# Optimization experiments

Measured on AMD Instinct MI355X. Metric: run time of the kernel, lower is better.

Reference implementation:

```python
import jax, jax.numpy as jnp
import numpy as np

NX = NY = 2048
DT = 0.01
DX = 1.0
DY = 1.0
RE = 1.0
NLEVEL = int(np.log2(NY)) + 1  # 12 levels


def pad_zero(x):
    # Dirichlet (zero) halo of width 1: matches boundary_condition_u/v/k/cw
    return jnp.pad(x, ((0, 0), (0, 0), (1, 1), (1, 1)))


def pad_edge(x):
    # Edge-replicate halo (incl. corners): matches boundary_condition_p
    return jnp.pad(x, ((0, 0), (0, 0), (1, 1), (1, 1)), mode='edge')


def conv2d(x, w, stride=1):
    return jax.lax.conv_general_dilated(
        x, w, (stride, stride), 'VALID',
        dimension_numbers=('NCHW', 'OIHW', 'NCHW'))


def upsample2(x):
    return jnp.repeat(jnp.repeat(x, 2, axis=2), 2, axis=3)


def pg_vector(u, v, pad_u, pad_v, k1, ADx_u, ADy_u, ADx_v, ADy_v, AD2_u, AD2_v, w_diff):
    # Petrov-Galerkin dissipation. pad_u/pad_v are the padded ORIGINAL velocities:
    # the torch code references the global values_uu/values_vv buffers here.
    k_u = 0.25 * DX * jnp.abs(0.5 * DX ** -3 * (jnp.abs(u) * DX + jnp.abs(v) * DY) * AD2_u) \
        / (0.001 + (jnp.abs(ADx_u) * DX ** -3 + jnp.abs(ADy_u) * DX ** -3) / 2.0)
    k_v = 0.25 * DY * jnp.abs(0.5 * DX ** -3 * (jnp.abs(u) * DX + jnp.abs(v) * DY) * AD2_v) \
        / (0.001 + (jnp.abs(ADx_v) * DX ** -3 + jnp.abs(ADy_v) * DX ** -3) / 2.0)
    k_u = jnp.minimum(k_u, k1)
    k_v = jnp.minimum(k_v, k1)
    k_uu = pad_zero(k_u)
    k_vv = pad_zero(k_v)
    k_x = 1.5 * (k_u * AD2_u + conv2d(pad_u * k_uu, w_diff) - u * conv2d(k_uu, w_diff))
    k_y = 1.5 * (k_v * AD2_v + conv2d(pad_v * k_vv, w_diff) - v * conv2d(k_vv, w_diff))
    return k_x, k_y


def f_cycle_mg(pad_u, pad_v, values_p, iteration, w_A, w_res, w_xadv, w_yadv):
    diag = w_A[0, 0, 1, 1]
    b = -(conv2d(pad_u, w_xadv) + conv2d(pad_v, w_yadv)) / DT
    w = jnp.zeros((1, 1, 2, 2), values_p.dtype)
    r = b
    for _ in range(iteration):
        w = jnp.zeros((1, 1, 2, 2), values_p.dtype)
        r = conv2d(pad_edge(values_p), w_A) - b
        r_s = [r]
        for _i in range(1, NLEVEL - 1):
            r = conv2d(r, w_res, stride=2)  # restriction down to 2x2
            r_s.append(r)
        for i in reversed(range(1, NLEVEL - 1)):
            w = w - conv2d(pad_zero(w), w_A) / diag + r_s[i] / diag  # Jacobi smooth
            w = upsample2(w)  # prolongation
        values_p = values_p - w
        values_p = values_p - conv2d(pad_edge(values_p), w_A) / diag + b / diag
    return values_p, w, r


def setup_inputs() -> dict:
    key = jax.random.key(0)
    ku, kv, kp = jax.random.split(key, 3)
    shp = (1, 1, NY, NX)
    f32 = jnp.float32
    values_u = jax.random.normal(ku, shp, f32) * 0.1
    values_v = jax.random.normal(kv, shp, f32) * 0.1
    values_p = jax.random.normal(kp, shp, f32) * 0.1
    Fx = jnp.zeros(shp, f32)
    Fy = jnp.zeros(shp, f32)
    k1 = jnp.ones(shp, f32) * (DX ** 2 / DT)
    # FD stencils (learned conv params in the torch module)
    w_xadv = jnp.array([[0., 0., 0.], [-0.5, 0., 0.5], [0., 0., 0.]], f32).reshape(1, 1, 3, 3) / DX
    w_yadv = jnp.array([[0., -0.5, 0.], [0., 0., 0.], [0., 0.5, 0.]], f32).reshape(1, 1, 3, 3) / DY
    lap = jnp.array([[0., 1., 0.], [1., -4., 1.], [0., 1., 0.]], f32).reshape(1, 1, 3, 3) / DX ** 2
    w_diff = lap
    w_A = lap  # diag = -4
    w_res = jnp.full((1, 1, 2, 2), 0.25, f32)
    return dict(values_u=values_u, values_v=values_v, values_p=values_p,
                Fx=Fx, Fy=Fy, k1=k1,
                w_xadv=w_xadv, w_yadv=w_yadv, w_diff=w_diff, w_A=w_A, w_res=w_res,
                iteration=5)


def reference(values_u, values_v, values_p, Fx, Fy, k1,
              w_xadv, w_yadv, w_diff, w_A, w_res, iteration):
    pad_u = pad_zero(values_u)
    pad_v = pad_zero(values_v)
    pad_p = pad_edge(values_p)
    Grapx_p = conv2d(pad_p, w_xadv) * DT
    Grapy_p = conv2d(pad_p, w_yadv) * DT
    ADx_u = conv2d(pad_u, w_xadv); ADy_u = conv2d(pad_u, w_yadv)
    ADx_v = conv2d(pad_v, w_xadv); ADy_v = conv2d(pad_v, w_yadv)
    AD2_u = conv2d(pad_u, w_diff); AD2_v = conv2d(pad_v, w_diff)
    k_x, k_y = pg_vector(values_u, values_v, pad_u, pad_v, k1,
                         ADx_u, ADy_u, ADx_v, ADy_v, AD2_u, AD2_v, w_diff)
    b_u = values_u + 0.5 * (RE * k_x * DT - values_u * ADx_u * DT - values_v * ADy_u * DT) - Grapx_p - Fx * DT * 0
    b_v = values_v + 0.5 * (RE * k_y * DT - values_u * ADx_v * DT - values_v * ADy_v * DT) - Grapy_p - Fy * DT * 0
    pad_bu = pad_zero(b_u)
    pad_bv = pad_zero(b_v)
    ADx_u = conv2d(pad_bu, w_xadv); ADy_u = conv2d(pad_bu, w_yadv)
    ADx_v = conv2d(pad_bv, w_xadv); ADy_v = conv2d(pad_bv, w_yadv)
    AD2_u = conv2d(pad_bu, w_diff); AD2_v = conv2d(pad_bv, w_diff)
    # torch code closes over the global padded ORIGINAL velocities here (pad_u, pad_v)
    k_x, k_y = pg_vector(b_u, b_v, pad_u, pad_v, k1,
                         ADx_u, ADy_u, ADx_v, ADy_v, AD2_u, AD2_v, w_diff)
    values_u = values_u + RE * k_x * DT - b_u * ADx_u * DT - b_v * ADy_u * DT - Grapx_p - Fx * DT
    values_v = values_v + RE * k_y * DT - b_u * ADx_v * DT - b_v * ADy_v * DT - Grapy_p - Fy * DT
    values_p, w, r = f_cycle_mg(pad_zero(values_u), pad_zero(values_v), values_p,
                                iteration, w_A, w_res, w_xadv, w_yadv)
    pad_p2 = pad_edge(values_p)
    values_u = values_u - conv2d(pad_p2, w_xadv) * DT
    values_v = values_v - conv2d(pad_p2, w_yadv) * DT
    return values_u, values_v, values_p, w, r
```

## Files before the change

kernel.cpp:

```cpp
#include <hip/hip_runtime.h>

#define NN 2048
#define NN2 (NN * NN)

__device__ __forceinline__ void load6z(const float* __restrict__ A, int i, int j0, float a[6]) {
    if ((unsigned)i >= (unsigned)NN) {
#pragma unroll
        for (int q = 0; q < 6; ++q) a[q] = 0.f;
        return;
    }
    const float* row = A + (size_t)i * NN;
    float4 c = *reinterpret_cast<const float4*>(row + j0);
    a[1] = c.x; a[2] = c.y; a[3] = c.z; a[4] = c.w;
    a[0] = (j0 > 0) ? row[j0 - 1] : 0.f;
    a[5] = (j0 + 4 < NN) ? row[j0 + 4] : 0.f;
}
__device__ __forceinline__ void load4z(const float* __restrict__ A, int i, int j0, float a[4]) {
    if ((unsigned)i >= (unsigned)NN) {
#pragma unroll
        for (int q = 0; q < 4; ++q) a[q] = 0.f;
        return;
    }
    float4 c = *reinterpret_cast<const float4*>(A + (size_t)i * NN + j0);
    a[0] = c.x; a[1] = c.y; a[2] = c.z; a[3] = c.w;
}
__device__ __forceinline__ void load6e(const float* __restrict__ A, int i, int j0, float a[6]) {
    i = i < 0 ? 0 : (i > NN - 1 ? NN - 1 : i);
    const float* row = A + (size_t)i * NN;
    float4 c = *reinterpret_cast<const float4*>(row + j0);
    a[1] = c.x; a[2] = c.y; a[3] = c.z; a[4] = c.w;
    a[0] = (j0 > 0) ? row[j0 - 1] : c.x;
    a[5] = (j0 + 4 < NN) ? row[j0 + 4] : c.w;
}
__device__ __forceinline__ void load4e(const float* __restrict__ A, int i, int j0, float a[4]) {
    i = i < 0 ? 0 : (i > NN - 1 ? NN - 1 : i);
    float4 c = *reinterpret_cast<const float4*>(A + (size_t)i * NN + j0);
    a[0] = c.x; a[1] = c.y; a[2] = c.z; a[3] = c.w;
}
__device__ __forceinline__ void store4(float* __restrict__ A, int i, int j0, const float a[4]) {
    *reinterpret_cast<float4*>(A + (size_t)i * NN + j0) = make_float4(a[0], a[1], a[2], a[3]);
}

__global__ __launch_bounds__(256) void k_pg1_v(const float* __restrict__ u, const float* __restrict__ v,
                                               const float* __restrict__ k1,
                                               float* __restrict__ ku, float* __restrict__ kv) {
    int jt = blockIdx.x * blockDim.x + threadIdx.x;
    int i  = blockIdx.y * blockDim.y + threadIdx.y;
    int j0 = jt * 4;
    float u6[6], v6[6], uu[4], ud[4], vu[4], vd[4], kc[4], oku[4], okv[4];
    load6z(u, i, j0, u6); load6z(v, i, j0, v6);
    load4z(u, i - 1, j0, uu); load4z(u, i + 1, j0, ud);
    load4z(v, i - 1, j0, vu); load4z(v, i + 1, j0, vd);
    load4z(k1, i, j0, kc);
#pragma unroll
    for (int c = 0; c < 4; ++c) {
        float uc = u6[c + 1], ul = u6[c], ur = u6[c + 2], ut = uu[c], ub = ud[c];
        float vc = v6[c + 1], vl = v6[c], vr = v6[c + 2], vt = vu[c], vb = vd[c];
        float ADxu = 0.5f * (ur - ul), ADyu = 0.5f * (ub - ut);
        float ADxv = 0.5f * (vr - vl), ADyv = 0.5f * (vb - vt);
        float Lu = ul + ur + ut + ub - 4.f * uc;
        float Lv = vl + vr + vt + vb - 4.f * vc;
        float s = fabsf(uc) + fabsf(vc);
        float kuv = 0.25f * fabsf(0.5f * s * Lu) / (0.001f + 0.5f * (fabsf(ADxu) + fabsf(ADyu)));
        float kvv = 0.25f * fabsf(0.5f * s * Lv) / (0.001f + 0.5f * (fabsf(ADxv) + fabsf(ADyv)));
        oku[c] = fminf(kuv, kc[c]); okv[c] = fminf(kvv, kc[c]);
    }
    store4(ku, i, j0, oku); store4(kv, i, j0, okv);
}

__global__ __launch_bounds__(256) void k_pred_v(const float* __restrict__ u, const float* __restrict__ v,
                                                const float* __restrict__ p,
                                                const float* __restrict__ ku, const float* __restrict__ kv,
                                                float* __restrict__ bu, float* __restrict__ bv) {
    const float DT = 0.01f;
    int jt = blockIdx.x * blockDim.x + threadIdx.x;
    int i  = blockIdx.y * blockDim.y + threadIdx.y;
    int j0 = jt * 4;
    float u6[6], v6[6], uu[4], ud[4], vu[4], vd[4];
    float ku6[6], kv6[6], kuu[4], kud[4], kvu[4], kvd[4];
    float p6[6], pu[4], pd[4], obu[4], obv[4];
    load6z(u, i, j0, u6); load6z(v, i, j0, v6);
    load4z(u, i - 1, j0, uu); load4z(u, i + 1, j0, ud);
    load4z(v, i - 1, j0, vu); load4z(v, i + 1, j0, vd);
    load6z(ku, i, j0, ku6); load6z(kv, i, j0, kv6);
    load4z(ku, i - 1, j0, kuu); load4z(ku, i + 1, j0, kud);
    load4z(kv, i - 1, j0, kvu); load4z(kv, i + 1, j0, kvd);
    load6e(p, i, j0, p6); load4e(p, i - 1, j0, pu); load4e(p, i + 1, j0, pd);
#pragma unroll
    for (int c = 0; c < 4; ++c) {
        float uc = u6[c + 1], ul = u6[c], ur = u6[c + 2], ut = uu[c], ub = ud[c];
        float vc = v6[c + 1], vl = v6[c], vr = v6[c + 2], vt = vu[c], vb = vd[c];
        float kuc = ku6[c + 1], kul = ku6[c], kur = ku6[c + 2], kut = kuu[c], kub = kud[c];
        float kvc = kv6[c + 1], kvl = kv6[c], kvr = kv6[c + 2], kvt = kvu[c], kvb = kvd[c];
        float ADxu = 0.5f * (ur - ul), ADyu = 0.5f * (ub - ut);
        float ADxv = 0.5f * (vr - vl), ADyv = 0.5f * (vb - vt);
        float Lu = ul + ur + ut + ub - 4.f * uc;
        float Lv = vl + vr + vt + vb - 4.f * vc;
        float Lku = kul + kur + kut + kub - 4.f * kuc;
        float Lkv = kvl + kvr + kvt + kvb - 4.f * kvc;
        float Luku = ul * kul + ur * kur + ut * kut + ub * kub - 4.f * uc * kuc;
        float Lvkv = vl * kvl + vr * kvr + vt * kvt + vb * kvb - 4.f * vc * kvc;
        float kx = 1.5f * (kuc * Lu + Luku - uc * Lku);
        float ky = 1.5f * (kvc * Lv + Lvkv - vc * Lkv);
        float Grapx = 0.5f * (p6[c + 2] - p6[c]) * DT;
        float Grapy = 0.5f * (pd[c] - pu[c]) * DT;
        obu[c] = uc + 0.5f * (kx * DT - uc * ADxu * DT - vc * ADyu * DT) - Grapx;
        obv[c] = vc + 0.5f * (ky * DT - uc * ADxv * DT - vc * ADyv * DT) - Grapy;
    }
    store4(bu, i, j0, obu); store4(bv, i, j0, obv);
}

__global__ __launch_bounds__(256) void k_corr_v(const float* __restrict__ u, const float* __restrict__ v,
                                                const float* __restrict__ p,
                                                const float* __restrict__ bu, const float* __restrict__ bv,
                                                const float* __restrict__ ku, const float* __restrict__ kv,
                                                const float* __restrict__ Fx, const float* __restrict__ Fy,
                                                float* __restrict__ un, float* __restrict__ vn) {
    const float DT = 0.01f;
    int jt = blockIdx.x * blockDim.x + threadIdx.x;
    int i  = blockIdx.y * blockDim.y + threadIdx.y;
    int j0 = jt * 4;
    float u6[6], v6[6], uu[4], ud[4], vu[4], vd[4];
    float bu6[6], bv6[6], buu[4], bud[4], bvu[4], bvd[4];
    float ku6[6], kv6[6], kuu[4], kud[4], kvu[4], kvd[4];
    float p6[6], pu[4], pd[4], fx[4], fy[4], oun[4], ovn[4];
    load6z(u, i, j0, u6); load6z(v, i, j0, v6);
    load4z(u, i - 1, j0, uu); load4z(u, i + 1, j0, ud);
    load4z(v, i - 1, j0, vu); load4z(v, i + 1, j0, vd);
    load6z(bu, i, j0, bu6); load6z(bv, i, j0, bv6);
    load4z(bu, i - 1, j0, buu); load4z(bu, i + 1, j0, bud);
    load4z(bv, i - 1, j0, bvu); load4z(bv, i + 1, j0, bvd);
    load6z(ku, i, j0, ku6); load6z(kv, i, j0, kv6);
    load4z(ku, i - 1, j0, kuu); load4z(ku, i + 1, j0, kud);
    load4z(kv, i - 1, j0, kvu); load4z(kv, i + 1, j0, kvd);
    load6e(p, i, j0, p6); load4e(p, i - 1, j0, pu); load4e(p, i + 1, j0, pd);
    load4z(Fx, i, j0, fx); load4z(Fy, i, j0, fy);
#pragma unroll
    for (int c = 0; c < 4; ++c) {
        float uc = u6[c + 1], ul = u6[c], ur = u6[c + 2], ut = uu[c], ub = ud[c];
        float vc = v6[c + 1], vl = v6[c], vr = v6[c + 2], vt = vu[c], vb = vd[c];
        float buc = bu6[c + 1], bul = bu6[c], bur = bu6[c + 2], but = buu[c], bub = bud[c];
        float bvc = bv6[c + 1], bvl = bv6[c], bvr = bv6[c + 2], bvt = bvu[c], bvb = bvd[c];
        float kuc = ku6[c + 1], kul = ku6[c], kur = ku6[c + 2], kut = kuu[c], kub = kud[c];
        float kvc = kv6[c + 1], kvl = kv6[c], kvr = kv6[c + 2], kvt = kvu[c], kvb = kvd[c];
        float ADxbu = 0.5f * (bur - bul), ADybu = 0.5f * (bub - but);
        float ADxbv = 0.5f * (bvr - bvl), ADybv = 0.5f * (bvb - bvt);
        float Lbu = bul + bur + but + bub - 4.f * buc;
        float Lbv = bvl + bvr + bvt + bvb - 4.f * bvc;
        float Lku = kul + kur + kut + kub - 4.f * kuc;
        float Lkv = kvl + kvr + kvt + kvb - 4.f * kvc;
        float Luku = ul * kul + ur * kur + ut * kut + ub * kub - 4.f * uc * kuc;
        float Lvkv = vl * kvl + vr * kvr + vt * kvt + vb * kvb - 4.f * vc * kvc;
        float kx = 1.5f * (kuc * Lbu + Luku - buc * Lku);
        float ky = 1.5f * (kvc * Lbv + Lvkv - bvc * Lkv);
        float Grapx = 0.5f * (p6[c + 2] - p6[c]) * DT;
        float Grapy = 0.5f * (pd[c] - pu[c]) * DT;
        oun[c] = uc + kx * DT - buc * ADxbu * DT - bvc * ADybu * DT - Grapx - fx[c] * DT;
        ovn[c] = vc + ky * DT - buc * ADxbv * DT - bvc * ADybv * DT - Grapy - fy[c] * DT;
    }
    store4(un, i, j0, oun); store4(vn, i, j0, ovn);
}

__global__ __launch_bounds__(256) void k_rhs_v(const float* __restrict__ un, const float* __restrict__ vn,
                                               float* __restrict__ b) {
    const float INVDT = 100.0f;
    int jt = blockIdx.x * blockDim.x + threadIdx.x;
    int i  = blockIdx.y * blockDim.y + threadIdx.y;
    int j0 = jt * 4;
    float u6[6], vu[4], vd[4], ob[4];
    load6z(un, i, j0, u6);
    load4z(vn, i - 1, j0, vu); load4z(vn, i + 1, j0, vd);
#pragma unroll
    for (int c = 0; c < 4; ++c) {
        float adx = 0.5f * (u6[c + 2] - u6[c]);
        float ady = 0.5f * (vd[c] - vu[c]);
        ob[c] = -(adx + ady) * INVDT;
    }
    store4(b, i, j0, ob);
}

__global__ __launch_bounds__(256) void k_resrestrict(const float* __restrict__ p, const float* __restrict__ b,
                                                     float* __restrict__ r1024, float* __restrict__ r512) {
    int jt = blockIdx.x * blockDim.x + threadIdx.x;
    int it = blockIdx.y * blockDim.y + threadIdx.y;
    int j0 = jt * 4, i0 = it * 4;
    float p6[6][6];
#pragma unroll
    for (int r = 0; r < 6; ++r) load6e(p, i0 - 1 + r, j0, p6[r]);
    float res[4][4];
#pragma unroll
    for (int r = 0; r < 4; ++r) {
        float bb[4];
        load4z(b, i0 + r, j0, bb);
#pragma unroll
        for (int c = 0; c < 4; ++c) {
            float pc = p6[r + 1][c + 1];
            float nb = p6[r][c + 1] + p6[r + 2][c + 1] + p6[r + 1][c] + p6[r + 1][c + 2];
            res[r][c] = nb - 4.f * pc - bb[c];
        }
    }
    float q00 = 0.25f * (res[0][0] + res[0][1] + res[1][0] + res[1][1]);
    float q01 = 0.25f * (res[0][2] + res[0][3] + res[1][2] + res[1][3]);
    float q10 = 0.25f * (res[2][0] + res[2][1] + res[3][0] + res[3][1]);
    float q11 = 0.25f * (res[2][2] + res[2][3] + res[3][2] + res[3][3]);
    int ci = it * 2, cj = jt * 2;
    *reinterpret_cast<float2*>(r1024 + (size_t)ci * 1024 + cj)       = make_float2(q00, q01);
    *reinterpret_cast<float2*>(r1024 + (size_t)(ci + 1) * 1024 + cj) = make_float2(q10, q11);
    r512[(size_t)it * 512 + jt] = 0.25f * (q00 + q01 + q10 + q11);
}

__global__ __launch_bounds__(256) void k_restrict2(const float* __restrict__ src,
                                                   float* __restrict__ dst1, float* __restrict__ dst2,
                                                   int n_src) {
    int j = blockIdx.x * blockDim.x + threadIdx.x;
    int i = blockIdx.y * blockDim.y + threadIdx.y;
    int n4 = n_src >> 2;
    int n2 = n_src >> 1;
    const float4* r0 = reinterpret_cast<const float4*>(src + (4 * i + 0) * n_src + 4 * j);
    const float4* r1 = reinterpret_cast<const float4*>(src + (4 * i + 1) * n_src + 4 * j);
    const float4* r2 = reinterpret_cast<const float4*>(src + (4 * i + 2) * n_src + 4 * j);
    const float4* r3 = reinterpret_cast<const float4*>(src + (4 * i + 3) * n_src + 4 * j);
    float4 a0 = *r0, a1 = *r1, a2 = *r2, a3 = *r3;
    float s00 = a0.x + a0.y + a1.x + a1.y;
    float s01 = a0.z + a0.w + a1.z + a1.w;
    float s10 = a2.x + a2.y + a3.x + a3.y;
    float s11 = a2.z + a2.w + a3.z + a3.w;
    *reinterpret_cast<float2*>(dst1 + (2 * i) * n2 + 2 * j)     = make_float2(0.25f * s00, 0.25f * s01);
    *reinterpret_cast<float2*>(dst1 + (2 * i + 1) * n2 + 2 * j) = make_float2(0.25f * s10, 0.25f * s11);
    dst2[i * n4 + j] = 0.0625f * (s00 + s01 + s10 + s11);
}

__global__ __launch_bounds__(1024) void k_small(const float* __restrict__ r128,
                                                float* __restrict__ w128_out,
                                                float* __restrict__ r2_out) {
    __shared__ float sr64[64 * 64];
    __shared__ float sr32[32 * 32];
    __shared__ float sr16[16 * 16];
    __shared__ float sr8[8 * 8];
    __shared__ float sr4[16];
    __shared__ float sr2[4];
    __shared__ float wa[64 * 64];
    __shared__ float wb[64 * 64];
    int t = threadIdx.x;

    for (int idx = t; idx < 64 * 64; idx += 1024) {
        int i = idx >> 6, j = idx & 63;
        const float* s0 = r128 + (2 * i) * 128 + 2 * j;
        sr64[idx] = 0.25f * (s0[0] + s0[1] + s0[128] + s0[129]);
    }
    __syncthreads();
    if (t < 32 * 32) {
        int i = t >> 5, j = t & 31;
        const float* s0 = sr64 + (2 * i) * 64 + 2 * j;
        sr32[t] = 0.25f * (s0[0] + s0[1] + s0[64] + s0[65]);
    }
    __syncthreads();
    if (t < 16 * 16) {
        int i = t >> 4, j = t & 15;
        const float* s0 = sr32 + (2 * i) * 32 + 2 * j;
        sr16[t] = 0.25f * (s0[0] + s0[1] + s0[32] + s0[33]);
    }
    __syncthreads();
    if (t < 64) {
        int i = t >> 3, j = t & 7;
        const float* s0 = sr16 + (2 * i) * 16 + 2 * j;
        sr8[t] = 0.25f * (s0[0] + s0[1] + s0[16] + s0[17]);
    }
    __syncthreads();
    if (t < 16) {
        int i = t >> 2, j = t & 3;
        const float* s0 = sr8 + (2 * i) * 8 + 2 * j;
        sr4[t] = 0.25f * (s0[0] + s0[1] + s0[8] + s0[9]);
    }
    __syncthreads();
    if (t < 4) {
        int i = t >> 1, j = t & 1;
        const float* s0 = sr4 + (2 * i) * 4 + 2 * j;
        sr2[t] = 0.25f * (s0[0] + s0[1] + s0[4] + s0[5]);
        r2_out[t] = sr2[t];
        float ws = -0.25f * sr2[t];
        wa[(2 * i) * 4 + 2 * j] = ws;
        wa[(2 * i) * 4 + 2 * j + 1] = ws;
        wa[(2 * i + 1) * 4 + 2 * j] = ws;
        wa[(2 * i + 1) * 4 + 2 * j + 1] = ws;
    }
    __syncthreads();

    auto step = [&](const float* win, const float* rl, float* wout, int s) {
        for (int idx = t; idx < s * s; idx += 1024) {
            int i = idx / s, j = idx - i * s;
            float up = i > 0 ? win[(i - 1) * s + j] : 0.f;
            float dn = i < s - 1 ? win[(i + 1) * s + j] : 0.f;
            float lf = j > 0 ? win[i * s + j - 1] : 0.f;
            float rt = j < s - 1 ? win[i * s + j + 1] : 0.f;
            float ws = 0.25f * (up + dn + lf + rt - rl[idx]);
            int o = 2 * s;
            wout[(2 * i) * o + 2 * j] = ws;
            wout[(2 * i) * o + 2 * j + 1] = ws;
            wout[(2 * i + 1) * o + 2 * j] = ws;
            wout[(2 * i + 1) * o + 2 * j + 1] = ws;
        }
    };
    step(wa, sr4, wb, 4);
    __syncthreads();
    step(wb, sr8, wa, 8);
    __syncthreads();
    step(wa, sr16, wb, 16);
    __syncthreads();
    step(wb, sr32, wa, 32);
    __syncthreads();
    step(wa, sr64, w128_out, 64);
}

__global__ __launch_bounds__(256) void k_prolong(const float* __restrict__ win, const float* __restrict__ rl,
                                                 float* __restrict__ wout, int n) {
    int j = blockIdx.x * blockDim.x + threadIdx.x;
    int i = blockIdx.y * blockDim.y + threadIdx.y;
    float up = i > 0 ? win[(i - 1) * n + j] : 0.f;
    float dn = i < n - 1 ? win[(i + 1) * n + j] : 0.f;
    float lf = j > 0 ? win[i * n + j - 1] : 0.f;
    float rt = j < n - 1 ? win[i * n + j + 1] : 0.f;
    float ws = 0.25f * (up + dn + lf + rt - rl[i * n + j]);
    int o = 2 * n;
    float2 vv = make_float2(ws, ws);
    *reinterpret_cast<float2*>(wout + (2 * i) * o + 2 * j) = vv;
    *reinterpret_cast<float2*>(wout + (2 * i + 1) * o + 2 * j) = vv;
}

template <bool LAST>
__global__ __launch_bounds__(256) void k_pupd_f(const float* __restrict__ p, const float* __restrict__ b,
                                                const float* __restrict__ w1024, const float* __restrict__ r1024,
                                                float* __restrict__ pdst, float* __restrict__ wout) {
    __shared__ float ws[4][130];
    const int jb = blockIdx.x * 256;
    const int ib = blockIdx.y * 4;
    const int cr_base = ib / 2 - 1;
    const int cc_base = jb / 2 - 1;
    const int tid = threadIdx.y * 64 + threadIdx.x;

    for (int cell = tid; cell < 4 * 130; cell += 256) {
        int r = cell / 130, c = cell - r * 130;
        int ci = cr_base + r, cj = cc_base + c;
        float val = 0.f;
        if ((unsigned)ci < 1024u && (unsigned)cj < 1024u) {
            const float* wr = w1024 + (size_t)ci * 1024;
            float up = ci > 0    ? wr[cj - 1024] : 0.f;
            float dn = ci < 1023 ? wr[cj + 1024] : 0.f;
            float lf = cj > 0    ? wr[cj - 1] : 0.f;
            float rt = cj < 1023 ? wr[cj + 1] : 0.f;
            val = 0.25f * (up + dn + lf + rt - r1024[(size_t)ci * 1024 + cj]);
        }
        ws[r][c] = val;
    }
    __syncthreads();

    const int i  = ib + threadIdx.y;
    const int j0 = jb + threadIdx.x * 4;
    float p6[6], pu[4], pd[4], bb[4], op[4];
    load6e(p, i, j0, p6);
    load4e(p, i - 1, j0, pu);
    load4e(p, i + 1, j0, pd);
    load4z(b, i, j0, bb);

    const int iu = (i - 1) < 0 ? 0 : (i - 1);
    const int id = (i + 1) > NN - 1 ? NN - 1 : (i + 1);
    const int lrC = (i >> 1) - cr_base;
    const int lrU = (iu >> 1) - cr_base;
    const int lrD = (id >> 1) - cr_base;

#pragma unroll
    for (int c = 0; c < 4; ++c) {
        int f = j0 + c;
        int fl = (f - 1) < 0 ? 0 : (f - 1);
        int fr = (f + 1) > NN - 1 ? NN - 1 : (f + 1);
        float pml = p6[c]     - ws[lrC][(fl >> 1) - cc_base];
        float pmr = p6[c + 2] - ws[lrC][(fr >> 1) - cc_base];
        float pmt = pu[c]     - ws[lrU][(f >> 1) - cc_base];
        float pmb = pd[c]     - ws[lrD][(f >> 1) - cc_base];
        op[c] = 0.25f * (pml + pmr + pmt + pmb - bb[c]);
    }
    store4(pdst, i, j0, op);
    if (LAST) {
        float ow[4];
#pragma unroll
        for (int c = 0; c < 4; ++c) ow[c] = ws[lrC][((j0 + c) >> 1) - cc_base];
        store4(wout, i, j0, ow);
    }
}

__global__ __launch_bounds__(256) void k_fcorr_v(const float* __restrict__ p,
                                                 float* __restrict__ un, float* __restrict__ vn) {
    const float DT = 0.01f;
    int jt = blockIdx.x * blockDim.x + threadIdx.x;
    int i  = blockIdx.y * blockDim.y + threadIdx.y;
    int j0 = jt * 4;
    float p6[6], pu[4], pd[4];
    load6e(p, i, j0, p6);
    load4e(p, i - 1, j0, pu);
    load4e(p, i + 1, j0, pd);
    float4 uc = *reinterpret_cast<float4*>(un + (size_t)i * NN + j0);
    float4 vc = *reinterpret_cast<float4*>(vn + (size_t)i * NN + j0);
    float ou[4] = {uc.x, uc.y, uc.z, uc.w};
    float ov[4] = {vc.x, vc.y, vc.z, vc.w};
#pragma unroll
    for (int c = 0; c < 4; ++c) {
        ou[c] -= 0.5f * (p6[c + 2] - p6[c]) * DT;
        ov[c] -= 0.5f * (pd[c] - pu[c]) * DT;
    }
    store4(un, i, j0, ou);
    store4(vn, i, j0, ov);
}

extern "C" void kernel_launch(void* const* d_in, const int* in_sizes, int n_in,
                              void* d_out, int out_size, void* d_ws, size_t ws_size,
                              hipStream_t stream) {
    const float* u  = (const float*)d_in[0];
    const float* v  = (const float*)d_in[1];
    const float* p  = (const float*)d_in[2];
    const float* Fx = (const float*)d_in[3];
    const float* Fy = (const float*)d_in[4];
    const float* k1 = (const float*)d_in[5];

    float* out = (float*)d_out;
    float* out_u = out;
    float* out_v = out + (size_t)NN2;
    float* out_p = out + 2 * (size_t)NN2;
    float* out_w = out + 3 * (size_t)NN2;
    float* out_r = out + 4 * (size_t)NN2;

    float* ws = (float*)d_ws;
    float* ku = ws;
    float* kv = ws + (size_t)NN2;
    float* b  = ws + 2 * (size_t)NN2;
    float* pA = ws + 3 * (size_t)NN2;
    float* pB = kv;
    float* r1024 = ws + 4 * (size_t)NN2;
    float* r512  = r1024 + 1024 * 1024;
    float* r256  = r512 + 512 * 512;
    float* r128  = r256 + 256 * 256;
    float* w128  = r128 + 128 * 128;
    float* w256  = w128 + 128 * 128;
    float* w512  = w256 + 256 * 256;
    float* w1024 = w512 + 512 * 512;

    float* bu = out_w;
    float* bv = out_p;

    dim3 blk(64, 4);
    dim3 g4(8, 512);

    k_pg1_v<<<g4, blk, 0, stream>>>(u, v, k1, ku, kv);
    k_pred_v<<<g4, blk, 0, stream>>>(u, v, p, ku, kv, bu, bv);
    k_pg1_v<<<g4, blk, 0, stream>>>(bu, bv, k1, ku, kv);
    k_corr_v<<<g4, blk, 0, stream>>>(u, v, p, bu, bv, ku, kv, Fx, Fy, out_u, out_v);
    k_rhs_v<<<g4, blk, 0, stream>>>(out_u, out_v, b);

    const float* pcur = p;
    for (int it = 0; it < 5; ++it) {
        k_resrestrict<<<dim3(8, 128), blk, 0, stream>>>(pcur, b, r1024, r512);
        k_restrict2<<<dim3(2, 32), blk, 0, stream>>>(r512, r256, r128, 512);
        k_small<<<1, 1024, 0, stream>>>(r128, w128, out_r);
        k_prolong<<<dim3(2, 32), blk, 0, stream>>>(w128, r128, w256, 128);
        k_prolong<<<dim3(4, 64), blk, 0, stream>>>(w256, r256, w512, 256);
        k_prolong<<<dim3(8, 128), blk, 0, stream>>>(w512, r512, w1024, 512);
        if (it < 4) {
            float* pdst = (it & 1) ? pB : pA;
            k_pupd_f<false><<<dim3(8, 512), blk, 0, stream>>>(pcur, b, w1024, r1024, pdst, nullptr);
            pcur = pdst;
        } else {
            k_pupd_f<true><<<dim3(8, 512), blk, 0, stream>>>(pcur, b, w1024, r1024, out_p, out_w);
        }
    }

    k_fcorr_v<<<g4, blk, 0, stream>>>(out_p, out_u, out_v);
}
```

Measured before the change: 425.7 us.

## Fuse PG dissipation into predictor/corrector and fold restriction and prolongation levels

Merges the two k_pg1 passes into the predictor and corrector kernels. Each block computes the limited diffusivity on a haloed shared-memory tile, so ku/kv no longer make a round trip through global memory. The 512→256→128 restriction is folded into the residual-restriction kernel using shared-memory reductions. The finest prolongation level is recomputed inside the pressure-update kernel from w512 and r512, removing the w1024 buffer. Together this drops several full-grid launches per cycle, at the cost of redundant halo computation, more shared memory per block and extra __syncthreads barriers.

```diff
diff --git a/kernel.cpp b/kernel.cpp
--- a/kernel.cpp
+++ b/kernel.cpp
@@ -41,124 +41,204 @@
     *reinterpret_cast<float4*>(A + (size_t)i * NN + j0) = make_float4(a[0], a[1], a[2], a[3]);
 }
 
-__global__ __launch_bounds__(256) void k_pg1_v(const float* __restrict__ u, const float* __restrict__ v,
-                                               const float* __restrict__ k1,
-                                               float* __restrict__ ku, float* __restrict__ kv) {
-    int jt = blockIdx.x * blockDim.x + threadIdx.x;
-    int i  = blockIdx.y * blockDim.y + threadIdx.y;
-    int j0 = jt * 4;
-    float u6[6], v6[6], uu[4], ud[4], vu[4], vd[4], kc[4], oku[4], okv[4];
-    load6z(u, i, j0, u6); load6z(v, i, j0, v6);
-    load4z(u, i - 1, j0, uu); load4z(u, i + 1, j0, ud);
-    load4z(v, i - 1, j0, vu); load4z(v, i + 1, j0, vd);
-    load4z(k1, i, j0, kc);
-#pragma unroll
-    for (int c = 0; c < 4; ++c) {
-        float uc = u6[c + 1], ul = u6[c], ur = u6[c + 2], ut = uu[c], ub = ud[c];
-        float vc = v6[c + 1], vl = v6[c], vr = v6[c + 2], vt = vu[c], vb = vd[c];
-        float ADxu = 0.5f * (ur - ul), ADyu = 0.5f * (ub - ut);
-        float ADxv = 0.5f * (vr - vl), ADyv = 0.5f * (vb - vt);
-        float Lu = ul + ur + ut + ub - 4.f * uc;
-        float Lv = vl + vr + vt + vb - 4.f * vc;
-        float s = fabsf(uc) + fabsf(vc);
-        float kuv = 0.25f * fabsf(0.5f * s * Lu) / (0.001f + 0.5f * (fabsf(ADxu) + fabsf(ADyu)));
-        float kvv = 0.25f * fabsf(0.5f * s * Lv) / (0.001f + 0.5f * (fabsf(ADxv) + fabsf(ADyv)));
-        oku[c] = fminf(kuv, kc[c]); okv[c] = fminf(kvv, kc[c]);
-    }
-    store4(ku, i, j0, oku); store4(kv, i, j0, okv);
-}
-
-__global__ __launch_bounds__(256) void k_pred_v(const float* __restrict__ u, const float* __restrict__ v,
-                                                const float* __restrict__ p,
-                                                const float* __restrict__ ku, const float* __restrict__ kv,
+__global__ __launch_bounds__(256) void k_pred_f(const float* __restrict__ u, const float* __restrict__ v,
+                                                const float* __restrict__ k1, const float* __restrict__ p,
                                                 float* __restrict__ bu, float* __restrict__ bv) {
     const float DT = 0.01f;
-    int jt = blockIdx.x * blockDim.x + threadIdx.x;
-    int i  = blockIdx.y * blockDim.y + threadIdx.y;
-    int j0 = jt * 4;
-    float u6[6], v6[6], uu[4], ud[4], vu[4], vd[4];
-    float ku6[6], kv6[6], kuu[4], kud[4], kvu[4], kvd[4];
-    float p6[6], pu[4], pd[4], obu[4], obv[4];
-    load6z(u, i, j0, u6); load6z(v, i, j0, v6);
-    load4z(u, i - 1, j0, uu); load4z(u, i + 1, j0, ud);
-    load4z(v, i - 1, j0, vu); load4z(v, i + 1, j0, vd);
-    load6z(ku, i, j0, ku6); load6z(kv, i, j0, kv6);
-    load4z(ku, i - 1, j0, kuu); load4z(ku, i + 1, j0, kud);
-    load4z(kv, i - 1, j0, kvu); load4z(kv, i + 1, j0, kvd);
-    load6e(p, i, j0, p6); load4e(p, i - 1, j0, pu); load4e(p, i + 1, j0, pd);
-#pragma unroll
-    for (int c = 0; c < 4; ++c) {
-        float uc = u6[c + 1], ul = u6[c], ur = u6[c + 2], ut = uu[c], ub = ud[c];
-        float vc = v6[c + 1], vl = v6[c], vr = v6[c + 2], vt = vu[c], vb = vd[c];
-        float kuc = ku6[c + 1], kul = ku6[c], kur = ku6[c + 2], kut = kuu[c], kub = kud[c];
-        float kvc = kv6[c + 1], kvl = kv6[c], kvr = kv6[c + 2], kvt = kvu[c], kvb = kvd[c];
-        float ADxu = 0.5f * (ur - ul), ADyu = 0.5f * (ub - ut);
-        float ADxv = 0.5f * (vr - vl), ADyv = 0.5f * (vb - vt);
-        float Lu = ul + ur + ut + ub - 4.f * uc;
-        float Lv = vl + vr + vt + vb - 4.f * vc;
-        float Lku = kul + kur + kut + kub - 4.f * kuc;
-        float Lkv = kvl + kvr + kvt + kvb - 4.f * kvc;
-        float Luku = ul * kul + ur * kur + ut * kut + ub * kub - 4.f * uc * kuc;
-        float Lvkv = vl * kvl + vr * kvr + vt * kvt + vb * kvb - 4.f * vc * kvc;
-        float kx = 1.5f * (kuc * Lu + Luku - uc * Lku);
-        float ky = 1.5f * (kvc * Lv + Lvkv - vc * Lkv);
-        float Grapx = 0.5f * (p6[c + 2] - p6[c]) * DT;
-        float Grapy = 0.5f * (pd[c] - pu[c]) * DT;
-        obu[c] = uc + 0.5f * (kx * DT - uc * ADxu * DT - vc * ADyu * DT) - Grapx;
-        obv[c] = vc + 0.5f * (ky * DT - uc * ADxv * DT - vc * ADyv * DT) - Grapy;
-    }
-    store4(bu, i, j0, obu); store4(bv, i, j0, obv);
-}
-
-__global__ __launch_bounds__(256) void k_corr_v(const float* __restrict__ u, const float* __restrict__ v,
-                                                const float* __restrict__ p,
+    __shared__ __align__(16) float su[36][72], sv[36][72];
+    __shared__ float sku[34][68], skv[34][68];
+    const int jb = blockIdx.x * 64;
+    const int ib = blockIdx.y * 32;
+    const int tid = threadIdx.y * 16 + threadIdx.x;
+
+    for (int idx = tid; idx < 36 * 18; idx += 256) {
+        int r = idx / 18, c4 = idx - r * 18;
+        int gi = ib - 2 + r;
+        int gj = jb - 4 + c4 * 4;
+        float4 uu = make_float4(0.f, 0.f, 0.f, 0.f), vv = uu;
+        if ((unsigned)gi < (unsigned)NN) {
+            if (gj >= 0 && gj + 3 < NN) {
+                uu = *reinterpret_cast<const float4*>(u + (size_t)gi * NN + gj);
+                vv = *reinterpret_cast<const float4*>(v + (size_t)gi * NN + gj);
+            } else {
+                float tu[4], tv[4];
+#pragma unroll
+                for (int q = 0; q < 4; ++q) {
+                    int g = gj + q;
+                    bool in = (unsigned)g < (unsigned)NN;
+                    tu[q] = in ? u[(size_t)gi * NN + g] : 0.f;
+                    tv[q] = in ? v[(size_t)gi * NN + g] : 0.f;
+                }
+                uu = make_float4(tu[0], tu[1], tu[2], tu[3]);
+                vv = make_float4(tv[0], tv[1], tv[2], tv[3]);
+            }
+        }
+        *reinterpret_cast<float4*>(&su[r][c4 * 4]) = uu;
+        *reinterpret_cast<float4*>(&sv[r][c4 * 4]) = vv;
+    }
+    __syncthreads();
+
+    for (int idx = tid; idx < 34 * 66; idx += 256) {
+        int r = idx / 66, c = idx - r * 66;
+        int gi = ib - 1 + r, gj = jb - 1 + c;
+        float kuo = 0.f, kvo = 0.f;
+        if ((unsigned)gi < (unsigned)NN && (unsigned)gj < (unsigned)NN) {
+            int lr = r + 1, lc = c + 3;
+            float uc = su[lr][lc], ul = su[lr][lc - 1], ur = su[lr][lc + 1], ut = su[lr - 1][lc], ub = su[lr + 1][lc];
+            float vc = sv[lr][lc], vl = sv[lr][lc - 1], vr = sv[lr][lc + 1], vt = sv[lr - 1][lc], vb = sv[lr + 1][lc];
+            float ADxu = 0.5f * (ur - ul), ADyu = 0.5f * (ub - ut);
+            float ADxv = 0.5f * (vr - vl), ADyv = 0.5f * (vb - vt);
+            float Lu = ul + ur + ut + ub - 4.f * uc;
+            float Lv = vl + vr + vt + vb - 4.f * vc;
+            float s = fabsf(uc) + fabsf(vc);
+            float kuv = 0.25f * fabsf(0.5f * s * Lu) / (0.001f + 0.5f * (fabsf(ADxu) + fabsf(ADyu)));
+            float kvv = 0.25f * fabsf(0.5f * s * Lv) / (0.001f + 0.5f * (fabsf(ADxv) + fabsf(ADyv)));
+            float k1c = k1[(size_t)gi * NN + gj];
+            kuo = fminf(kuv, k1c);
+            kvo = fminf(kvv, k1c);
+        }
+        sku[r][c] = kuo;
+        skv[r][c] = kvo;
+    }
+    __syncthreads();
+
+    const int i0 = ib + threadIdx.y * 2;
+    const int j0 = jb + threadIdx.x * 4;
+#pragma unroll
+    for (int a = 0; a < 2; ++a) {
+        int i = i0 + a;
+        float p6[6], pu[4], pd[4], obu[4], obv[4];
+        load6e(p, i, j0, p6); load4e(p, i - 1, j0, pu); load4e(p, i + 1, j0, pd);
+        int lur = i - ib + 2, lkr = i - ib + 1;
+#pragma unroll
+        for (int c = 0; c < 4; ++c) {
+            int luc = j0 + c - jb + 4, lkc = j0 + c - jb + 1;
+            float uc = su[lur][luc], ul = su[lur][luc - 1], ur = su[lur][luc + 1], ut = su[lur - 1][luc], ub = su[lur + 1][luc];
+            float vc = sv[lur][luc], vl = sv[lur][luc - 1], vr = sv[lur][luc + 1], vt = sv[lur - 1][luc], vb = sv[lur + 1][luc];
+            float kuc = sku[lkr][lkc], kul = sku[lkr][lkc - 1], kur = sku[lkr][lkc + 1], kut = sku[lkr - 1][lkc], kub = sku[lkr + 1][lkc];
+            float kvc = skv[lkr][lkc], kvl = skv[lkr][lkc - 1], kvr = skv[lkr][lkc + 1], kvt = skv[lkr - 1][lkc], kvb = skv[lkr + 1][lkc];
+            float ADxu = 0.5f * (ur - ul), ADyu = 0.5f * (ub - ut);
+            float ADxv = 0.5f * (vr - vl), ADyv = 0.5f * (vb - vt);
+            float Lu = ul + ur + ut + ub - 4.f * uc;
+            float Lv = vl + vr + vt + vb - 4.f * vc;
+            float Lku = kul + kur + kut + kub - 4.f * kuc;
+            float Lkv = kvl + kvr + kvt + kvb - 4.f * kvc;
+            float Luku = ul * kul + ur * kur + ut * kut + ub * kub - 4.f * uc * kuc;
+            float Lvkv = vl * kvl + vr * kvr + vt * kvt + vb * kvb - 4.f * vc * kvc;
+            float kx = 1.5f * (kuc * Lu + Luku - uc * Lku);
+            float ky = 1.5f * (kvc * Lv + Lvkv - vc * Lkv);
+            float Grapx = 0.5f * (p6[c + 2] - p6[c]) * DT;
+            float Grapy = 0.5f * (pd[c] - pu[c]) * DT;
+            obu[c] = uc + 0.5f * (kx * DT - uc * ADxu * DT - vc * ADyu * DT) - Grapx;
+            obv[c] = vc + 0.5f * (ky * DT - uc * ADxv * DT - vc * ADyv * DT) - Grapy;
+        }
+        store4(bu, i, j0, obu);
+        store4(bv, i, j0, obv);
+    }
+}
+
+__global__ __launch_bounds__(256) void k_corr_f(const float* __restrict__ u, const float* __restrict__ v,
+                                                const float* __restrict__ k1, const float* __restrict__ p,
                                                 const float* __restrict__ bu, const float* __restrict__ bv,
-                                                const float* __restrict__ ku, const float* __restrict__ kv,
                                                 const float* __restrict__ Fx, const float* __restrict__ Fy,
                                                 float* __restrict__ un, float* __restrict__ vn) {
     const float DT = 0.01f;
-    int jt = blockIdx.x * blockDim.x + threadIdx.x;
-    int i  = blockIdx.y * blockDim.y + threadIdx.y;
-    int j0 = jt * 4;
-    float u6[6], v6[6], uu[4], ud[4], vu[4], vd[4];
-    float bu6[6], bv6[6], buu[4], bud[4], bvu[4], bvd[4];
-    float ku6[6], kv6[6], kuu[4], kud[4], kvu[4], kvd[4];
-    float p6[6], pu[4], pd[4], fx[4], fy[4], oun[4], ovn[4];
-    load6z(u, i, j0, u6); load6z(v, i, j0, v6);
-    load4z(u, i - 1, j0, uu); load4z(u, i + 1, j0, ud);
-    load4z(v, i - 1, j0, vu); load4z(v, i + 1, j0, vd);
-    load6z(bu, i, j0, bu6); load6z(bv, i, j0, bv6);
-    load4z(bu, i - 1, j0, buu); load4z(bu, i + 1, j0, bud);
-    load4z(bv, i - 1, j0, bvu); load4z(bv, i + 1, j0, bvd);
-    load6z(ku, i, j0, ku6); load6z(kv, i, j0, kv6);
-    load4z(ku, i - 1, j0, kuu); load4z(ku, i + 1, j0, kud);
-    load4z(kv, i - 1, j0, kvu); load4z(kv, i + 1, j0, kvd);
-    load6e(p, i, j0, p6); load4e(p, i - 1, j0, pu); load4e(p, i + 1, j0, pd);
-    load4z(Fx, i, j0, fx); load4z(Fy, i, j0, fy);
-#pragma unroll
-    for (int c = 0; c < 4; ++c) {
-        float uc = u6[c + 1], ul = u6[c], ur = u6[c + 2], ut = uu[c], ub = ud[c];
-        float vc = v6[c + 1], vl = v6[c], vr = v6[c + 2], vt = vu[c], vb = vd[c];
-        float buc = bu6[c + 1], bul = bu6[c], bur = bu6[c + 2], but = buu[c], bub = bud[c];
-        float bvc = bv6[c + 1], bvl = bv6[c], bvr = bv6[c + 2], bvt = bvu[c], bvb = bvd[c];
-        float kuc = ku6[c + 1], kul = ku6[c], kur = ku6[c + 2], kut = kuu[c], kub = kud[c];
-        float kvc = kv6[c + 1], kvl = kv6[c], kvr = kv6[c + 2], kvt = kvu[c], kvb = kvd[c];
-        float ADxbu = 0.5f * (bur - bul), ADybu = 0.5f * (bub - but);
-        float ADxbv = 0.5f * (bvr - bvl), ADybv = 0.5f * (bvb - bvt);
-        float Lbu = bul + bur + but + bub - 4.f * buc;
-        float Lbv = bvl + bvr + bvt + bvb - 4.f * bvc;
-        float Lku = kul + kur + kut + kub - 4.f * kuc;
-        float Lkv = kvl + kvr + kvt + kvb - 4.f * kvc;
-        float Luku = ul * kul + ur * kur + ut * kut + ub * kub - 4.f * uc * kuc;
-        float Lvkv = vl * kvl + vr * kvr + vt * kvt + vb * kvb - 4.f * vc * kvc;
-        float kx = 1.5f * (kuc * Lbu + Luku - buc * Lku);
-        float ky = 1.5f * (kvc * Lbv + Lvkv - bvc * Lkv);
-        float Grapx = 0.5f * (p6[c + 2] - p6[c]) * DT;
-        float Grapy = 0.5f * (pd[c] - pu[c]) * DT;
-        oun[c] = uc + kx * DT - buc * ADxbu * DT - bvc * ADybu * DT - Grapx - fx[c] * DT;
-        ovn[c] = vc + ky * DT - buc * ADxbv * DT - bvc * ADybv * DT - Grapy - fy[c] * DT;
-    }
-    store4(un, i, j0, oun); store4(vn, i, j0, ovn);
+    __shared__ __align__(16) float sbu[36][72], sbv[36][72];
+    __shared__ float sku[34][68], skv[34][68];
+    const int jb = blockIdx.x * 64;
+    const int ib = blockIdx.y * 32;
+    const int tid = threadIdx.y * 16 + threadIdx.x;
+
+    for (int idx = tid; idx < 36 * 18; idx += 256) {
+        int r = idx / 18, c4 = idx - r * 18;
+        int gi = ib - 2 + r;
+        int gj = jb - 4 + c4 * 4;
+        float4 uu = make_float4(0.f, 0.f, 0.f, 0.f), vv = uu;
+        if ((unsigned)gi < (unsigned)NN) {
+            if (gj >= 0 && gj + 3 < NN) {
+                uu = *reinterpret_cast<const float4*>(bu + (size_t)gi * NN + gj);
+                vv = *reinterpret_cast<const float4*>(bv + (size_t)gi * NN + gj);
+            } else {
+                float tu[4], tv[4];
+#pragma unroll
+                for (int q = 0; q < 4; ++q) {
+                    int g = gj + q;
+                    bool in = (unsigned)g < (unsigned)NN;
+                    tu[q] = in ? bu[(size_t)gi * NN + g] : 0.f;
+                    tv[q] = in ? bv[(size_t)gi * NN + g] : 0.f;
+                }
+                uu = make_float4(tu[0], tu[1], tu[2], tu[3]);
+                vv = make_float4(tv[0], tv[1], tv[2], tv[3]);
+            }
+        }
+        *reinterpret_cast<float4*>(&sbu[r][c4 * 4]) = uu;
+        *reinterpret_cast<float4*>(&sbv[r][c4 * 4]) = vv;
+    }
+    __syncthreads();
+
+    for (int idx = tid; idx < 34 * 66; idx += 256) {
+        int r = idx / 66, c = idx - r * 66;
+        int gi = ib - 1 + r, gj = jb - 1 + c;
+        float kuo = 0.f, kvo = 0.f;
+        if ((unsigned)gi < (unsigned)NN && (unsigned)gj < (unsigned)NN) {
+            int lr = r + 1, lc = c + 3;
+            float uc = sbu[lr][lc], ul = sbu[lr][lc - 1], ur = sbu[lr][lc + 1], ut = sbu[lr - 1][lc], ub = sbu[lr + 1][lc];
+            float vc = sbv[lr][lc], vl = sbv[lr][lc - 1], vr = sbv[lr][lc + 1], vt = sbv[lr - 1][lc], vb = sbv[lr + 1][lc];
+            float ADxu = 0.5f * (ur - ul), ADyu = 0.5f * (ub - ut);
+            float ADxv = 0.5f * (vr - vl), ADyv = 0.5f * (vb - vt);
+            float Lu = ul + ur + ut + ub - 4.f * uc;
+            float Lv = vl + vr + vt + vb - 4.f * vc;
+            float s = fabsf(uc) + fabsf(vc);
+            float kuv = 0.25f * fabsf(0.5f * s * Lu) / (0.001f + 0.5f * (fabsf(ADxu) + fabsf(ADyu)));
+            float kvv = 0.25f * fabsf(0.5f * s * Lv) / (0.001f + 0.5f * (fabsf(ADxv) + fabsf(ADyv)));
+            float k1c = k1[(size_t)gi * NN + gj];
+            kuo = fminf(kuv, k1c);
+            kvo = fminf(kvv, k1c);
+        }
+        sku[r][c] = kuo;
+        skv[r][c] = kvo;
+    }
+    __syncthreads();
+
+    const int i0 = ib + threadIdx.y * 2;
+    const int j0 = jb + threadIdx.x * 4;
+#pragma unroll
+    for (int a = 0; a < 2; ++a) {
+        int i = i0 + a;
+        float p6[6], pu[4], pd[4];
+        float u6[6], uu[4], ud[4], v6[6], vu[4], vd[4], fx[4], fy[4], oun[4], ovn[4];
+        load6e(p, i, j0, p6); load4e(p, i - 1, j0, pu); load4e(p, i + 1, j0, pd);
+        load6z(u, i, j0, u6); load4z(u, i - 1, j0, uu); load4z(u, i + 1, j0, ud);
+        load6z(v, i, j0, v6); load4z(v, i - 1, j0, vu); load4z(v, i + 1, j0, vd);
+        load4z(Fx, i, j0, fx); load4z(Fy, i, j0, fy);
+        int lbr = i - ib + 2, lkr = i - ib + 1;
+#pragma unroll
+        for (int c = 0; c < 4; ++c) {
+            int lbc = j0 + c - jb + 4, lkc = j0 + c - jb + 1;
+            float buc = sbu[lbr][lbc], bul = sbu[lbr][lbc - 1], bur = sbu[lbr][lbc + 1], but = sbu[lbr - 1][lbc], bub = sbu[lbr + 1][lbc];
+            float bvc = sbv[lbr][lbc], bvl = sbv[lbr][lbc - 1], bvr = sbv[lbr][lbc + 1], bvt = sbv[lbr - 1][lbc], bvb = sbv[lbr + 1][lbc];
+            float kuc = sku[lkr][lkc], kul = sku[lkr][lkc - 1], kur = sku[lkr][lkc + 1], kut = sku[lkr - 1][lkc], kub = sku[lkr + 1][lkc];
+            float kvc = skv[lkr][lkc], kvl = skv[lkr][lkc - 1], kvr = skv[lkr][lkc + 1], kvt = skv[lkr - 1][lkc], kvb = skv[lkr + 1][lkc];
+            float uc = u6[c + 1], ul = u6[c], ur = u6[c + 2], ut = uu[c], ub = ud[c];
+            float vc = v6[c + 1], vl = v6[c], vr = v6[c + 2], vt = vu[c], vb = vd[c];
+            float ADxbu = 0.5f * (bur - bul), ADybu = 0.5f * (bub - but);
+            float ADxbv = 0.5f * (bvr - bvl), ADybv = 0.5f * (bvb - bvt);
+            float Lbu = bul + bur + but + bub - 4.f * buc;
+            float Lbv = bvl + bvr + bvt + bvb - 4.f * bvc;
+            float Lku = kul + kur + kut + kub - 4.f * kuc;
+            float Lkv = kvl + kvr + kvt + kvb - 4.f * kvc;
+            float Luku = ul * kul + ur * kur + ut * kut + ub * kub - 4.f * uc * kuc;
+            float Lvkv = vl * kvl + vr * kvr + vt * kvt + vb * kvb - 4.f * vc * kvc;
+            float kx = 1.5f * (kuc * Lbu + Luku - buc * Lku);
+            float ky = 1.5f * (kvc * Lbv + Lvkv - bvc * Lkv);
+            float Grapx = 0.5f * (p6[c + 2] - p6[c]) * DT;
+            float Grapy = 0.5f * (pd[c] - pu[c]) * DT;
+            oun[c] = uc + kx * DT - buc * ADxbu * DT - bvc * ADybu * DT - Grapx - fx[c] * DT;
+            ovn[c] = vc + ky * DT - buc * ADxbv * DT - bvc * ADybv * DT - Grapy - fy[c] * DT;
+        }
+        store4(un, i, j0, oun);
+        store4(vn, i, j0, ovn);
+    }
 }
 
 __global__ __launch_bounds__(256) void k_rhs_v(const float* __restrict__ un, const float* __restrict__ vn,
@@ -180,9 +260,13 @@
 }
 
 __global__ __launch_bounds__(256) void k_resrestrict(const float* __restrict__ p, const float* __restrict__ b,
-                                                     float* __restrict__ r1024, float* __restrict__ r512) {
-    int jt = blockIdx.x * blockDim.x + threadIdx.x;
-    int it = blockIdx.y * blockDim.y + threadIdx.y;
+                                                     float* __restrict__ r1024, float* __restrict__ r512,
+                                                     float* __restrict__ r256, float* __restrict__ r128) {
+    __shared__ float s512[4][64];
+    __shared__ float s256[2][32];
+    int tx = threadIdx.x, ty = threadIdx.y;
+    int jt = blockIdx.x * 64 + tx;
+    int it = blockIdx.y * 4 + ty;
     int j0 = jt * 4, i0 = it * 4;
     float p6[6][6];
 #pragma unroll
@@ -206,28 +290,22 @@
     int ci = it * 2, cj = jt * 2;
     *reinterpret_cast<float2*>(r1024 + (size_t)ci * 1024 + cj)       = make_float2(q00, q01);
     *reinterpret_cast<float2*>(r1024 + (size_t)(ci + 1) * 1024 + cj) = make_float2(q10, q11);
-    r512[(size_t)it * 512 + jt] = 0.25f * (q00 + q01 + q10 + q11);
-}
-
-__global__ __launch_bounds__(256) void k_restrict2(const float* __restrict__ src,
-                                                   float* __restrict__ dst1, float* __restrict__ dst2,
-                                                   int n_src) {
-    int j = blockIdx.x * blockDim.x + threadIdx.x;
-    int i = blockIdx.y * blockDim.y + threadIdx.y;
-    int n4 = n_src >> 2;
-    int n2 = n_src >> 1;
-    const float4* r0 = reinterpret_cast<const float4*>(src + (4 * i + 0) * n_src + 4 * j);
-    const float4* r1 = reinterpret_cast<const float4*>(src + (4 * i + 1) * n_src + 4 * j);
-    const float4* r2 = reinterpret_cast<const float4*>(src + (4 * i + 2) * n_src + 4 * j);
-    const float4* r3 = reinterpret_cast<const float4*>(src + (4 * i + 3) * n_src + 4 * j);
-    float4 a0 = *r0, a1 = *r1, a2 = *r2, a3 = *r3;
-    float s00 = a0.x + a0.y + a1.x + a1.y;
-    float s01 = a0.z + a0.w + a1.z + a1.w;
-    float s10 = a2.x + a2.y + a3.x + a3.y;
-    float s11 = a2.z + a2.w + a3.z + a3.w;
-    *reinterpret_cast<float2*>(dst1 + (2 * i) * n2 + 2 * j)     = make_float2(0.25f * s00, 0.25f * s01);
-    *reinterpret_cast<float2*>(dst1 + (2 * i + 1) * n2 + 2 * j) = make_float2(0.25f * s10, 0.25f * s11);
-    dst2[i * n4 + j] = 0.0625f * (s00 + s01 + s10 + s11);
+    float s = 0.25f * (q00 + q01 + q10 + q11);
+    r512[(size_t)it * 512 + jt] = s;
+    s512[ty][tx] = s;
+    __syncthreads();
+    int tid = ty * 64 + tx;
+    if (tid < 64) {
+        int a = tid >> 5, c = tid & 31;
+        float m = 0.25f * (s512[2 * a][2 * c] + s512[2 * a][2 * c + 1] + s512[2 * a + 1][2 * c] + s512[2 * a + 1][2 * c + 1]);
+        r256[(size_t)(blockIdx.y * 2 + a) * 256 + blockIdx.x * 32 + c] = m;
+        s256[a][c] = m;
+    }
+    __syncthreads();
+    if (tid < 16) {
+        float m = 0.25f * (s256[0][2 * tid] + s256[0][2 * tid + 1] + s256[1][2 * tid] + s256[1][2 * tid + 1]);
+        r128[(size_t)blockIdx.y * 128 + blockIdx.x * 16 + tid] = m;
+    }
 }
 
 __global__ __launch_bounds__(1024) void k_small(const float* __restrict__ r128,
@@ -328,27 +406,63 @@
 }
 
 template <bool LAST>
-__global__ __launch_bounds__(256) void k_pupd_f(const float* __restrict__ p, const float* __restrict__ b,
-                                                const float* __restrict__ w1024, const float* __restrict__ r1024,
-                                                float* __restrict__ pdst, float* __restrict__ wout) {
+__global__ __launch_bounds__(256) void k_pupd2(const float* __restrict__ p, const float* __restrict__ b,
+                                               const float* __restrict__ w512, const float* __restrict__ r512,
+                                               const float* __restrict__ r1024,
+                                               float* __restrict__ pdst, float* __restrict__ wout) {
+    __shared__ float sW[6][72];
+    __shared__ float sS[4][68];
     __shared__ float ws[4][130];
     const int jb = blockIdx.x * 256;
     const int ib = blockIdx.y * 4;
     const int cr_base = ib / 2 - 1;
     const int cc_base = jb / 2 - 1;
+    const int sr_base = (ib / 2 - 2) >> 1;
+    const int sc_base = (jb / 2 - 2) >> 1;
+    const int wr_base = sr_base - 1, wc_base = sc_base - 1;
     const int tid = threadIdx.y * 64 + threadIdx.x;
 
-    for (int cell = tid; cell < 4 * 130; cell += 256) {
-        int r = cell / 130, c = cell - r * 130;
+    for (int idx = tid; idx < 6 * 68; idx += 256) {
+        int r = idx / 68, c = idx - r * 68;
+        int gi = wr_base + r, gj = wc_base + c;
+        sW[r][c] = ((unsigned)gi < 512u && (unsigned)gj < 512u) ? w512[(size_t)gi * 512 + gj] : 0.f;
+    }
+    __syncthreads();
+    for (int idx = tid; idx < 4 * 66; idx += 256) {
+        int r = idx / 66, c = idx - r * 66;
+        int gi = sr_base + r, gj = sc_base + c;
+        float val = 0.f;
+        if ((unsigned)gi < 512u && (unsigned)gj < 512u) {
+            int lr = r + 1, lc = c + 1;
+            val = 0.25f * (sW[lr - 1][lc] + sW[lr + 1][lc] + sW[lr][lc - 1] + sW[lr][lc + 1]
+                           - r512[(size_t)gi * 512 + gj]);
+        }
+        sS[r][c] = val;
+    }
+    __syncthreads();
+    for (int idx = tid; idx < 4 * 130; idx += 256) {
+        int r = idx / 130, c = idx - r * 130;
         int ci = cr_base + r, cj = cc_base + c;
         float val = 0.f;
         if ((unsigned)ci < 1024u && (unsigned)cj < 1024u) {
-            const float* wr = w1024 + (size_t)ci * 1024;
-            float up = ci > 0    ? wr[cj - 1024] : 0.f;
-            float dn = ci < 1023 ? wr[cj + 1024] : 0.f;
-            float lf = cj > 0    ? wr[cj - 1] : 0.f;
-            float rt = cj < 1023 ? wr[cj + 1] : 0.f;
-            val = 0.25f * (up + dn + lf + rt - r1024[(size_t)ci * 1024 + cj]);
+            float nsum = 0.f;
+            {
+                int R = ci - 1, C = cj;
+                if ((unsigned)R < 1024u) nsum += sS[(R >> 1) - sr_base][(C >> 1) - sc_base];
+            }
+            {
+                int R = ci + 1, C = cj;
+                if ((unsigned)R < 1024u) nsum += sS[(R >> 1) - sr_base][(C >> 1) - sc_base];
+            }
+            {
+                int R = ci, C = cj - 1;
+                if ((unsigned)C < 1024u) nsum += sS[(R >> 1) - sr_base][(C >> 1) - sc_base];
+            }
+            {
+                int R = ci, C = cj + 1;
+                if ((unsigned)C < 1024u) nsum += sS[(R >> 1) - sr_base][(C >> 1) - sc_base];
+            }
+            val = 0.25f * (nsum - r1024[(size_t)ci * 1024 + cj]);
         }
         ws[r][c] = val;
     }
@@ -429,46 +543,41 @@
     float* out_r = out + 4 * (size_t)NN2;
 
     float* ws = (float*)d_ws;
-    float* ku = ws;
-    float* kv = ws + (size_t)NN2;
-    float* b  = ws + 2 * (size_t)NN2;
-    float* pA = ws + 3 * (size_t)NN2;
-    float* pB = kv;
-    float* r1024 = ws + 4 * (size_t)NN2;
+    float* b  = ws;
+    float* pA = ws + (size_t)NN2;
+    float* pB = ws + 2 * (size_t)NN2;
+    float* r1024 = ws + 3 * (size_t)NN2;
     float* r512  = r1024 + 1024 * 1024;
     float* r256  = r512 + 512 * 512;
     float* r128  = r256 + 256 * 256;
     float* w128  = r128 + 128 * 128;
     float* w256  = w128 + 128 * 128;
     float* w512  = w256 + 256 * 256;
-    float* w1024 = w512 + 512 * 512;
 
     float* bu = out_w;
     float* bv = out_p;
 
     dim3 blk(64, 4);
     dim3 g4(8, 512);
-
-    k_pg1_v<<<g4, blk, 0, stream>>>(u, v, k1, ku, kv);
-    k_pred_v<<<g4, blk, 0, stream>>>(u, v, p, ku, kv, bu, bv);
-    k_pg1_v<<<g4, blk, 0, stream>>>(bu, bv, k1, ku, kv);
-    k_corr_v<<<g4, blk, 0, stream>>>(u, v, p, bu, bv, ku, kv, Fx, Fy, out_u, out_v);
+    dim3 blkT(16, 16);
+    dim3 gT(32, 64);
+
+    k_pred_f<<<gT, blkT, 0, stream>>>(u, v, k1, p, bu, bv);
+    k_corr_f<<<gT, blkT, 0, stream>>>(u, v, k1, p, bu, bv, Fx, Fy, out_u, out_v);
     k_rhs_v<<<g4, blk, 0, stream>>>(out_u, out_v, b);
 
     const float* pcur = p;
     for (int it = 0; it < 5; ++it) {
-        k_resrestrict<<<dim3(8, 128), blk, 0, stream>>>(pcur, b, r1024, r512);
-        k_restrict2<<<dim3(2, 32), blk, 0, stream>>>(r512, r256, r128, 512);
+        k_resrestrict<<<dim3(8, 128), blk, 0, stream>>>(pcur, b, r1024, r512, r256, r128);
         k_small<<<1, 1024, 0, stream>>>(r128, w128, out_r);
         k_prolong<<<dim3(2, 32), blk, 0, stream>>>(w128, r128, w256, 128);
         k_prolong<<<dim3(4, 64), blk, 0, stream>>>(w256, r256, w512, 256);
-        k_prolong<<<dim3(8, 128), blk, 0, stream>>>(w512, r512, w1024, 512);
         if (it < 4) {
             float* pdst = (it & 1) ? pB : pA;
-            k_pupd_f<false><<<dim3(8, 512), blk, 0, stream>>>(pcur, b, w1024, r1024, pdst, nullptr);
+            k_pupd2<false><<<dim3(8, 512), blk, 0, stream>>>(pcur, b, w512, r512, r1024, pdst, nullptr);
             pcur = pdst;
         } else {
-            k_pupd_f<true><<<dim3(8, 512), blk, 0, stream>>>(pcur, b, w1024, r1024, out_p, out_w);
+            k_pupd2<true><<<dim3(8, 512), blk, 0, stream>>>(pcur, b, w512, r512, r1024, out_p, out_w);
         }
     }
 
```

Result: faster. 400.8 us (-5.9%).
